# Performance work log

Measured on AMD Instinct MI355X. Metric: run time of the kernel, lower is better.

Reference implementation:

```python
import jax, jax.numpy as jnp
import numpy as np

N, E, C = 100000, 50000, 256
M, D, F, T = 128, 128, 128, 64
MSG = 2 * D + F + T  # 448
T_MAX = 100000


def setup_inputs() -> dict:
    key = jax.random.key(0)
    ks = jax.random.split(key, 16)
    src = jax.random.randint(ks[0], (E,), 0, N, dtype=jnp.int32)
    dst = jax.random.randint(ks[1], (E,), 0, N, dtype=jnp.int32)
    t = jnp.sort(jax.random.randint(ks[2], (E,), 0, T_MAX, dtype=jnp.int32))
    last_update = jax.random.randint(ks[3], (N,), 0, 1000, dtype=jnp.int32)
    event_feat = jax.random.normal(ks[4], (E, F), dtype=jnp.float32)
    src_embeds = jax.random.normal(ks[5], (E, D), dtype=jnp.float32)
    dst_embeds = jax.random.normal(ks[6], (E, D), dtype=jnp.float32)
    nodes_memory = jax.random.normal(ks[7], (N, M), dtype=jnp.float32)
    incidence = jax.random.uniform(ks[8], (N, C), dtype=jnp.float32)
    w_time = jax.random.normal(ks[9], (T,), dtype=jnp.float32)
    b_time = jax.random.normal(ks[10], (T,), dtype=jnp.float32)
    W_ih = jax.random.normal(ks[11], (MSG, 3 * M), dtype=jnp.float32) * 0.05
    W_hh = jax.random.normal(ks[12], (M, 3 * M), dtype=jnp.float32) * 0.05
    b_ih = jnp.zeros((3 * M,), jnp.float32)
    b_hh = jnp.zeros((3 * M,), jnp.float32)
    return dict(src=src, dst=dst, t=t, last_update=last_update,
                event_feat=event_feat, src_embeds=src_embeds, dst_embeds=dst_embeds,
                nodes_memory=nodes_memory, incidence=incidence,
                w_time=w_time, b_time=b_time, W_ih=W_ih, W_hh=W_hh,
                b_ih=b_ih, b_hh=b_hh)


def reference(src, dst, t, last_update, event_feat, src_embeds, dst_embeds,
              nodes_memory, incidence, w_time, b_time, W_ih, W_hh, b_ih, b_hh):
    E2 = 2 * E
    # store_events: raw messages + flipped-direction messages, keyed by source node
    src_all = jnp.concatenate([src, dst])            # [2E]
    emb_s = jnp.concatenate([src_embeds, dst_embeds], axis=0)
    emb_d = jnp.concatenate([dst_embeds, src_embeds], axis=0)
    feat = jnp.concatenate([event_feat, event_feat], axis=0)
    t_all = jnp.concatenate([t, t])                  # [2E]
    # message function: concat(src_embed, dst_embed, event_feat, time_encoding(dt))
    dt = (t_all - last_update[src_all]).astype(jnp.float32)
    time_enc = jnp.cos(dt[:, None] * w_time[None, :] + b_time[None, :])  # [2E, T]
    msg = jnp.concatenate([emb_s, emb_d, feat, time_enc], axis=-1)       # [2E, MSG]
    # 'last' aggregation: per-node argmax over timestamps via rank-encoded segment_max
    perm = jnp.argsort(t_all)  # ascending time order
    rank = jnp.zeros((E2,), jnp.int32).at[perm].set(jnp.arange(E2, dtype=jnp.int32))
    seg_rank = jax.ops.segment_max(rank, src_all, num_segments=N)
    counts = jax.ops.segment_sum(jnp.ones((E2,), jnp.int32), src_all, num_segments=N)
    has_msg = counts > 0                              # [N]
    last_idx = perm[jnp.where(has_msg, seg_rank, 0)]  # [N] event index of last message
    agg_msg = msg[last_idx]                           # [N, MSG]
    # GRU memory updater (torch.nn.GRUCell convention)
    gx = agg_msg @ W_ih + b_ih
    gh = nodes_memory @ W_hh + b_hh
    xr, xz, xn = jnp.split(gx, 3, axis=-1)
    hr, hz, hn = jnp.split(gh, 3, axis=-1)
    r = jax.nn.sigmoid(xr + hr)
    z = jax.nn.sigmoid(xz + hz)
    n = jnp.tanh(xn + r * hn)
    h_new = (1.0 - z) * n + z * nodes_memory
    new_mem = jnp.where(has_msg[:, None], h_new, nodes_memory)  # [N, M]
    # rewire_graph: community memory = incidence.T @ nodes_memory
    comm_mem = jnp.einsum('nc,nm->cm', incidence, new_mem)      # [C, M]
    return jnp.concatenate([new_mem, comm_mem], axis=0)         # [N + C, M]
```

## Files before the change

### kernel.cpp

```cpp
#include <hip/hip_runtime.h>
#include <hip/hip_bf16.h>
#include <stdint.h>

#define N_NODES   100000
#define N_EVENTS  50000
#define N_COMM    256
#define DIM_M     128
#define K_TOT     576
#define GCOLS     512
#define INV2PI    0.15915494309189535f

typedef float f32x4 __attribute__((ext_vector_type(4)));
typedef short s16x8 __attribute__((ext_vector_type(8)));
typedef short s16x4 __attribute__((ext_vector_type(4)));

#define KEYS_OFF   0
#define CNT_OFF    800000
#define LIST_OFF   800008
#define W2PI_OFF   1200128
#define B2PI_OFF   1200384
#define WT_OFF     1200640
#define X_ROWS     100096
#define X_OFF      1790464
#define PART_M_OFF X_OFF
#define CT_NCH     256
#define CT_CPN     392
#define TMP2_OFF   (PART_M_OFF + 33554432)
#define TENC_OFF   1790464
#define PART_F_OFF 14594560

__device__ inline unsigned short f2bf(float x) {
    union { float f; unsigned u; } v; v.f = x;
    unsigned r = v.u + 0x7FFFu + ((v.u >> 16) & 1u);
    return (unsigned short)(r >> 16);
}
__device__ inline float bf2f(unsigned short u) {
    union { unsigned u; float f; } v; v.u = ((unsigned)u) << 16;
    return v.f;
}
__device__ inline float cos_rev(float rev) {
    float fr = rev - floorf(rev);
#if __has_builtin(__builtin_amdgcn_cosf)
    return __builtin_amdgcn_cosf(fr);
#else
    return cosf(fr * 6.283185307179586f);
#endif
}
__device__ inline float sigmoid_f(float x) { return 1.0f / (1.0f + __expf(-x)); }
__device__ inline float tanh_f(float x) {
    float t = __expf(2.0f * x);
    return 1.0f - 2.0f / (t + 1.0f);
}

__global__ __launch_bounds__(256) void k_agg(const int* __restrict__ src,
                                             const int* __restrict__ dst,
                                             const int* __restrict__ t,
                                             unsigned long long* __restrict__ keys) {
    int i = blockIdx.x * 256 + threadIdx.x;
    if (i >= 2 * N_EVENTS) return;
    int e = (i < N_EVENTS) ? i : i - N_EVENTS;
    int node = (i < N_EVENTS) ? src[i] : dst[e];
    unsigned long long key =
        ((unsigned long long)(unsigned)t[e] << 32) | (unsigned)(i + 1);
    atomicMax(&keys[node], key);
}

__global__ __launch_bounds__(256) void k_compact(const unsigned long long* __restrict__ keys,
                                                 unsigned int* __restrict__ cnt,
                                                 int* __restrict__ list) {
    int n = blockIdx.x * 256 + threadIdx.x;
    if (n >= N_NODES) return;
    if (keys[n] != 0ULL) {
        unsigned p = atomicAdd(cnt, 1u);
        list[p] = n;
    }
}

__global__ void k_prep(const float* __restrict__ w_time, const float* __restrict__ b_time,
                       float* __restrict__ w2, float* __restrict__ b2) {
    int i = threadIdx.x;
    if (i < 64) { w2[i] = w_time[i] * INV2PI; b2[i] = b_time[i] * INV2PI; }
}

__global__ __launch_bounds__(256) void k_wconv(const float* __restrict__ W_ih,
                                               const float* __restrict__ W_hh,
                                               unsigned short* __restrict__ Wt) {
    int idx = blockIdx.x * 256 + threadIdx.x;
    if (idx >= GCOLS * K_TOT) return;
    int col2 = idx / K_TOT, k = idx % K_TOT;
    int mh = col2 >> 8, rem = col2 & 255;
    int g = rem >> 6, m = mh * 64 + (rem & 63);
    float v;
    if (g == 0)      v = (k < 448) ? W_ih[(size_t)k * 384 + m]
                                   : W_hh[(size_t)(k - 448) * 384 + m];
    else if (g == 1) v = (k < 448) ? W_ih[(size_t)k * 384 + 128 + m]
                                   : W_hh[(size_t)(k - 448) * 384 + 128 + m];
    else if (g == 2) v = (k < 448) ? W_ih[(size_t)k * 384 + 256 + m] : 0.0f;
    else             v = (k < 448) ? 0.0f : W_hh[(size_t)(k - 448) * 384 + 256 + m];
    Wt[idx] = f2bf(v);
}

__global__ __launch_bounds__(256) void k_wconv_old(const float* __restrict__ W_ih,
                                                   const float* __restrict__ W_hh,
                                                   unsigned short* __restrict__ Wt) {
    int idx = blockIdx.x * 256 + threadIdx.x;
    if (idx >= GCOLS * K_TOT) return;
    int col = idx / K_TOT, k = idx % K_TOT;
    float v;
    if (col < 256) {
        v = (k < 448) ? W_ih[(size_t)k * 384 + col]
                      : W_hh[(size_t)(k - 448) * 384 + col];
    } else if (col < 384) {
        v = (k < 448) ? W_ih[(size_t)k * 384 + col] : 0.0f;
    } else {
        v = (k < 448) ? 0.0f : W_hh[(size_t)(k - 448) * 384 + (col - 128)];
    }
    Wt[idx] = f2bf(v);
}

__global__ __launch_bounds__(256) void k_xbuild(
    const unsigned long long* __restrict__ keys,
    const unsigned int* __restrict__ cnt,
    const int* __restrict__ list,
    const int* __restrict__ t,
    const int* __restrict__ last_update,
    const float* __restrict__ event_feat,
    const float* __restrict__ src_embeds,
    const float* __restrict__ dst_embeds,
    const float* __restrict__ mem,
    const float* __restrict__ w2pi,
    const float* __restrict__ b2pi,
    unsigned short* __restrict__ X) {
    const unsigned c = *cnt;
    const unsigned cpad = (c + 127u) & ~127u;
    const unsigned total = cpad * 72u;
    for (unsigned idx = blockIdx.x * 256 + threadIdx.x; idx < total;
         idx += gridDim.x * 256) {
        const unsigned row = idx / 72u;
        const int s = (int)(idx - row * 72u);
        unsigned short* xp = X + (size_t)row * K_TOT + s * 8;
        s16x8 v;
        if (row >= c) {
#pragma unroll
            for (int j = 0; j < 8; ++j) v[j] = 0;
            *(s16x8*)xp = v;
            continue;
        }
        const int node = list[row];
        const unsigned long long key = keys[node];
        const int ia = (int)(key & 0xffffffffull) - 1;
        const int e = (ia < N_EVENTS) ? ia : ia - N_EVENTS;
        if (s < 48) {
            const float* p;
            if (s < 16)
                p = ((ia < N_EVENTS) ? src_embeds : dst_embeds) + (size_t)e * 128 + s * 8;
            else if (s < 32)
                p = ((ia < N_EVENTS) ? dst_embeds : src_embeds) + (size_t)e * 128 + (s - 16) * 8;
            else
                p = event_feat + (size_t)e * 128 + (s - 32) * 8;
            float4 a = *(const float4*)p;
            float4 b = *(const float4*)(p + 4);
            v[0] = (short)f2bf(a.x); v[1] = (short)f2bf(a.y);
            v[2] = (short)f2bf(a.z); v[3] = (short)f2bf(a.w);
            v[4] = (short)f2bf(b.x); v[5] = (short)f2bf(b.y);
            v[6] = (short)f2bf(b.z); v[7] = (short)f2bf(b.w);
        } else if (s < 56) {
            const float dt = (float)(t[e] - last_update[node]);
            const int c0 = (s - 48) * 8;
#pragma unroll
            for (int j = 0; j < 8; ++j) {
                float rev = fmaf(dt, w2pi[c0 + j], b2pi[c0 + j]);
                v[j] = (short)f2bf(cos_rev(rev));
            }
        } else {
            const float* p = mem + (size_t)node * 128 + (s - 56) * 8;
            float4 a = *(const float4*)p;
            float4 b = *(const float4*)(p + 4);
            v[0] = (short)f2bf(a.x); v[1] = (short)f2bf(a.y);
            v[2] = (short)f2bf(a.z); v[3] = (short)f2bf(a.w);
            v[4] = (short)f2bf(b.x); v[5] = (short)f2bf(b.y);
            v[6] = (short)f2bf(b.z); v[7] = (short)f2bf(b.w);
        }
        *(s16x8*)xp = v;
    }
}

__global__ __launch_bounds__(512, 4) void k_gemm2(
    const unsigned int* __restrict__ cnt,
    const int* __restrict__ list,
    const unsigned short* __restrict__ X,
    const unsigned short* __restrict__ Wt,
    const float* __restrict__ b_ih,
    const float* __restrict__ b_hh,
    float* __restrict__ out) {
    __shared__ unsigned short Xs[3][128][64];
    __shared__ int Ls[128];

    const unsigned c = *cnt;
    const int rb = blockIdx.x >> 1;
    const int mh = blockIdx.x & 1;
    const int base = rb * 128;
    if ((unsigned)base >= c) return;
    const int tid = threadIdx.x;
    const int w = tid >> 6, l = tid & 63;
    const int lr = l & 15, lk = l >> 4;
    const int wm = w >> 2, wn = w & 3;

    if (tid < 128)
        Ls[tid] = ((unsigned)(base + tid) < c) ? list[base + tid] : 0;

    const int sroff = l >> 3;
    const int sslot = ((l & 7) ^ sroff) << 3;
    const unsigned short* gsrc0 =
        X + (size_t)(base + w * 16 + sroff) * K_TOT + sslot;

    auto stage = [&](int ch, int buf) {
        __builtin_amdgcn_global_load_lds(
            (const __attribute__((address_space(1))) unsigned int*)(gsrc0 + ch * 64),
            (__attribute__((address_space(3))) unsigned int*)&Xs[buf][w * 16][0],
            16, 0, 0);
        __builtin_amdgcn_global_load_lds(
            (const __attribute__((address_space(1))) unsigned int*)(gsrc0 + 8 * K_TOT + ch * 64),
            (__attribute__((address_space(3))) unsigned int*)&Xs[buf][w * 16 + 8][0],
            16, 0, 0);
    };

    f32x4 acc[4][4];
#pragma unroll
    for (int rt = 0; rt < 4; ++rt)
#pragma unroll
        for (int i = 0; i < 4; ++i) acc[rt][i] = (f32x4){0.f, 0.f, 0.f, 0.f};

    stage(0, 0);
    stage(1, 1);
    asm volatile("s_waitcnt vmcnt(2)" ::: "memory");
    __builtin_amdgcn_s_barrier();

    int buf = 0;
    for (int ch = 0; ch < 9; ++ch) {
        __builtin_amdgcn_s_setprio(1);
#pragma unroll
        for (int ks = 0; ks < 2; ++ks) {
            s16x8 a[4];
#pragma unroll
            for (int rt = 0; rt < 4; ++rt) {
                const int r = wm * 64 + rt * 16 + lr;
                const int sl = (ks * 4 + lk) ^ (r & 7);
                a[rt] = *(const s16x8*)&Xs[buf][r][sl << 3];
            }
#pragma unroll
            for (int i = 0; i < 4; ++i) {
                const int col2 = mh * 256 + i * 64 + wn * 16 + lr;
                s16x8 b = *(const s16x8*)&Wt[(size_t)col2 * K_TOT + ch * 64 + ks * 32 + lk * 8];
#pragma unroll
                for (int rt = 0; rt < 4; ++rt)
                    acc[rt][i] = __builtin_amdgcn_mfma_f32_16x16x32_bf16(
                        a[rt], b, acc[rt][i], 0, 0, 0);
            }
        }
        __builtin_amdgcn_s_setprio(0);
        if (ch <= 6) {
            int nbuf = buf + 2; if (nbuf >= 3) nbuf -= 3;
            stage(ch + 2, nbuf);
        }
        if (ch < 8) {
            __builtin_amdgcn_sched_barrier(0);
            if (ch < 7) asm volatile("s_waitcnt vmcnt(2)" ::: "memory");
            else        asm volatile("s_waitcnt vmcnt(0)" ::: "memory");
            __builtin_amdgcn_s_barrier();
            __builtin_amdgcn_sched_barrier(0);
        }
        if (++buf == 3) buf = 0;
    }

    const int mcol = mh * 64 + wn * 16 + lr;
    const float b_r  = b_ih[mcol] + b_hh[mcol];
    const float b_z  = b_ih[128 + mcol] + b_hh[128 + mcol];
    const float b_xn = b_ih[256 + mcol];
    const float b_hn = b_hh[256 + mcol];
    const int hbuf = (mcol < 64) ? 1 : 2;
    const int kk   = (mcol < 64) ? mcol : mcol - 64;
#pragma unroll
    for (int rt = 0; rt < 4; ++rt) {
#pragma unroll
        for (int reg = 0; reg < 4; ++reg) {
            const int r = wm * 64 + rt * 16 + lk * 4 + reg;
            const int grow = base + r;
            if ((unsigned)grow < c) {
                const int node = Ls[r];
                const float h = bf2f(Xs[hbuf][r][(((kk >> 3) ^ (r & 7)) << 3) + (kk & 7)]);
                float rr = sigmoid_f(acc[rt][0][reg] + b_r);
                float zz = sigmoid_f(acc[rt][1][reg] + b_z);
                float nn = tanh_f(acc[rt][2][reg] + b_xn + rr * (acc[rt][3][reg] + b_hn));
                out[(size_t)node * 128 + mcol] = (1.0f - zz) * nn + zz * h;
            }
        }
    }
}

__global__ __launch_bounds__(256) void k_copy(const unsigned long long* __restrict__ keys,
                                              const float* __restrict__ nm,
                                              float* __restrict__ out) {
    int idx = blockIdx.x * 256 + threadIdx.x;
    int n = idx >> 5;
    if (n >= N_NODES) return;
    if (keys[n] != 0ULL) return;
    ((float4*)out)[idx] = ((const float4*)nm)[idx];
}

__global__ __launch_bounds__(512) void k_comm_t(const float* __restrict__ inc,
                                                const float* __restrict__ nm,
                                                float* __restrict__ partials) {
    __shared__ unsigned short T[2][12288];

    const int bid = blockIdx.x;
    const int n0 = bid * CT_CPN;
    const int n1 = min(N_NODES, n0 + CT_CPN);
    const int ng = (n1 - n0 + 31) >> 5;
    const int tid = threadIdx.x;
    const int w = tid >> 6, l = tid & 63;
    const int lr = l & 15, lk = l >> 4;

    float vi[4][4];
    float vm[4][2];

    auto load_chunk = [&](int g) {
        const int nb = n0 + g * 32 + w * 4;
#pragma unroll
        for (int ri = 0; ri < 4; ++ri) {
            const int n = nb + ri;
            const bool ok = n < n1;
#pragma unroll
            for (int j = 0; j < 4; ++j)
                vi[ri][j] = ok ? inc[(size_t)n * N_COMM + l + 64 * j] : 0.0f;
#pragma unroll
            for (int j = 0; j < 2; ++j)
                vm[ri][j] = ok ? nm[(size_t)n * DIM_M + l + 64 * j] : 0.0f;
        }
    };
    auto write_chunk = [&](int buf) {
        unsigned short* bi = &T[buf][0];
#pragma unroll
        for (int j = 0; j < 4; ++j) {
            const int cc = l + 64 * j;
            ushort4 p = make_ushort4(f2bf(vi[0][j]), f2bf(vi[1][j]),
                                     f2bf(vi[2][j]), f2bf(vi[3][j]));
            *(ushort4*)&bi[cc * 32 + ((w ^ (cc & 7)) << 2)] = p;
        }
        unsigned short* bm = &T[buf][8192];
#pragma unroll
        for (int j = 0; j < 2; ++j) {
            const int mm = l + 64 * j;
            ushort4 p = make_ushort4(f2bf(vm[0][j]), f2bf(vm[1][j]),
                                     f2bf(vm[2][j]), f2bf(vm[3][j]));
            *(ushort4*)&bm[mm * 32 + ((w ^ (mm & 7)) << 2)] = p;
        }
    };

    f32x4 acc[2][8];
#pragma unroll
    for (int ct = 0; ct < 2; ++ct)
#pragma unroll
        for (int mt = 0; mt < 8; ++mt) acc[ct][mt] = (f32x4){0.f, 0.f, 0.f, 0.f};

    auto compute_chunk = [&](int buf) {
        const unsigned short* bi = &T[buf][0];
        const unsigned short* bm = &T[buf][8192];
        s16x8 a[2];
#pragma unroll
        for (int ct = 0; ct < 2; ++ct) {
            const int cc = (w * 2 + ct) * 16 + lr;
            s16x4 lo = *(const s16x4*)&bi[cc * 32 + (((lk * 2) ^ (cc & 7)) << 2)];
            s16x4 hi = *(const s16x4*)&bi[cc * 32 + (((lk * 2 + 1) ^ (cc & 7)) << 2)];
            a[ct] = __builtin_shufflevector(lo, hi, 0, 1, 2, 3, 4, 5, 6, 7);
        }
#pragma unroll
        for (int mt = 0; mt < 8; ++mt) {
            const int mm = mt * 16 + lr;
            s16x4 lo = *(const s16x4*)&bm[mm * 32 + (((lk * 2) ^ (mm & 7)) << 2)];
            s16x4 hi = *(const s16x4*)&bm[mm * 32 + (((lk * 2 + 1) ^ (mm & 7)) << 2)];
            s16x8 b = __builtin_shufflevector(lo, hi, 0, 1, 2, 3, 4, 5, 6, 7);
            acc[0][mt] = __builtin_amdgcn_mfma_f32_16x16x32_bf16(a[0], b, acc[0][mt], 0, 0, 0);
            acc[1][mt] = __builtin_amdgcn_mfma_f32_16x16x32_bf16(a[1], b, acc[1][mt], 0, 0, 0);
        }
    };

    load_chunk(0);
    write_chunk(0);
    __syncthreads();
    for (int g = 0; g < ng; ++g) {
        if (g + 1 < ng) load_chunk(g + 1);
        compute_chunk(g & 1);
        if (g + 1 < ng) write_chunk((g + 1) & 1);
        __syncthreads();
    }

    float* p = partials + (size_t)bid * (N_COMM * DIM_M);
#pragma unroll
    for (int ct = 0; ct < 2; ++ct) {
#pragma unroll
        for (int mt = 0; mt < 8; ++mt) {
#pragma unroll
            for (int reg = 0; reg < 4; ++reg) {
                const int cc = (w * 2 + ct) * 16 + lk * 4 + reg;
                p[(size_t)cc * DIM_M + mt * 16 + lr] = acc[ct][mt][reg];
            }
        }
    }
}

__global__ __launch_bounds__(256) void k_comm2a(const float* __restrict__ partials,
                                                float* __restrict__ tmp) {
    const int bid = blockIdx.x;
    const int y = bid >> 5, x = bid & 31;
    const int idx4 = x * 256 + threadIdx.x;
    float4 s = make_float4(0.f, 0.f, 0.f, 0.f);
    for (int ci = 0; ci < CT_NCH / 16; ++ci) {
        float4 v = *(const float4*)&partials[(size_t)(y * (CT_NCH / 16) + ci) * (N_COMM * DIM_M) + idx4 * 4];
        s.x += v.x; s.y += v.y; s.z += v.z; s.w += v.w;
    }
    *(float4*)&tmp[(size_t)y * (N_COMM * DIM_M) + idx4 * 4] = s;
}

__global__ __launch_bounds__(256) void k_comm2b(const float* __restrict__ tmp,
                                                float* __restrict__ out) {
    const int idx4 = blockIdx.x * 256 + threadIdx.x;
    float4 s = make_float4(0.f, 0.f, 0.f, 0.f);
    for (int y = 0; y < 16; ++y) {
        float4 v = *(const float4*)&tmp[(size_t)y * (N_COMM * DIM_M) + idx4 * 4];
        s.x += v.x; s.y += v.y; s.z += v.z; s.w += v.w;
    }
    *(float4*)&out[(size_t)N_NODES * DIM_M + idx4 * 4] = s;
}

__global__ __launch_bounds__(256) void k_tenc(const unsigned long long* __restrict__ keys,
                                              const unsigned int* __restrict__ cnt,
                                              const int* __restrict__ list,
                                              const int* __restrict__ t,
                                              const int* __restrict__ last_update,
                                              const float* __restrict__ w_time,
                                              const float* __restrict__ b_time,
                                              unsigned short* __restrict__ tenc) {
    int idx = blockIdx.x * 256 + threadIdx.x;
    int r = idx >> 3, slot = idx & 7;
    const unsigned c = *cnt;
    const unsigned cpad = (c + 63u) & ~63u;
    if ((unsigned)r >= cpad) return;
    s16x8 v;
    if ((unsigned)r < c) {
        int node = list[r];
        unsigned long long key = keys[node];
        int ia = (int)(key & 0xffffffffull) - 1;
        int e = (ia < N_EVENTS) ? ia : ia - N_EVENTS;
        float dt = (float)(t[e] - last_update[node]);
#pragma unroll
        for (int j = 0; j < 8; ++j) {
            int cix = slot * 8 + j;
            float arg = __fadd_rn(__fmul_rn(dt, w_time[cix]), b_time[cix]);
            v[j] = (short)f2bf(cosf(arg));
        }
    } else {
#pragma unroll
        for (int j = 0; j < 8; ++j) v[j] = 0;
    }
    *(s16x8*)&tenc[(size_t)r * 64 + slot * 8] = v;
}

__global__ __launch_bounds__(256, 2) void k_gemm_fused(
    const unsigned long long* __restrict__ keys,
    const unsigned int* __restrict__ cnt,
    const int* __restrict__ list,
    const float* __restrict__ event_feat,
    const float* __restrict__ src_embeds,
    const float* __restrict__ dst_embeds,
    const float* __restrict__ mem,
    const unsigned short* __restrict__ tenc,
    const unsigned short* __restrict__ Wt,
    const float* __restrict__ b_ih,
    const float* __restrict__ b_hh,
    float* __restrict__ out) {
    __shared__ unsigned short Xs[2][4][64][8];

    const unsigned c = *cnt;
    const int base = blockIdx.x * 64;
    if ((unsigned)base >= c) return;
    const int tid = threadIdx.x;

    const int srow = tid >> 2;
    const int kslot = tid & 3;
    const int sgrow = base + srow;
    const bool valid = (unsigned)sgrow < c;
    const float *p_es = nullptr, *p_ed = nullptr, *p_ef = nullptr, *p_mem = nullptr;
    const unsigned short* p_te = nullptr;
    if (valid) {
        int node = list[sgrow];
        unsigned long long key = keys[node];
        int ia = (int)(key & 0xffffffffull) - 1;
        int e = (ia < N_EVENTS) ? ia : ia - N_EVENTS;
        const float* sp = src_embeds + (size_t)e * 128;
        const float* dp = dst_embeds + (size_t)e * 128;
        p_es = (ia < N_EVENTS) ? sp : dp;
        p_ed = (ia < N_EVENTS) ? dp : sp;
        p_ef = event_feat + (size_t)e * 128;
        p_te = tenc + (size_t)sgrow * 64;
        p_mem = mem + (size_t)node * 128;
    }

    auto stage = [&](int ch) {
        const int buf = ch & 1;
        const int k0 = ch * 32 + kslot * 8;
        s16x8 v;
        if (valid) {
            if (k0 < 384) {
                const float* p = (k0 < 128) ? (p_es + k0)
                               : (k0 < 256) ? (p_ed + (k0 - 128))
                                            : (p_ef + (k0 - 256));
                float4 a = *(const float4*)p;
                float4 b = *(const float4*)(p + 4);
                v[0] = (short)f2bf(a.x); v[1] = (short)f2bf(a.y);
                v[2] = (short)f2bf(a.z); v[3] = (short)f2bf(a.w);
                v[4] = (short)f2bf(b.x); v[5] = (short)f2bf(b.y);
                v[6] = (short)f2bf(b.z); v[7] = (short)f2bf(b.w);
            } else if (k0 < 448) {
                v = *(const s16x8*)(p_te + (k0 - 384));
            } else {
                const float* p = p_mem + (k0 - 448);
                float4 a = *(const float4*)p;
                float4 b = *(const float4*)(p + 4);
                v[0] = (short)f2bf(a.x); v[1] = (short)f2bf(a.y);
                v[2] = (short)f2bf(a.z); v[3] = (short)f2bf(a.w);
                v[4] = (short)f2bf(b.x); v[5] = (short)f2bf(b.y);
                v[6] = (short)f2bf(b.z); v[7] = (short)f2bf(b.w);
            }
        } else {
#pragma unroll
            for (int j = 0; j < 8; ++j) v[j] = 0;
        }
        *(s16x8*)&Xs[buf][kslot][srow][0] = v;
    };

    const int w = tid >> 6;
    const int l = tid & 63;
    const int lr = l & 15;
    const int lk = l >> 4;

    f32x4 acc[4][8];
#pragma unroll
    for (int rt = 0; rt < 4; ++rt)
#pragma unroll
        for (int i = 0; i < 8; ++i) acc[rt][i] = (f32x4){0.f, 0.f, 0.f, 0.f};

    stage(0);
    __syncthreads();

    for (int ch = 0; ch < 18; ++ch) {
        if (ch < 17) stage(ch + 1);
        const int buf = ch & 1;
        s16x8 a[4];
#pragma unroll
        for (int rt = 0; rt < 4; ++rt)
            a[rt] = *(const s16x8*)&Xs[buf][lk][rt * 16 + lr][0];
#pragma unroll
        for (int i = 0; i < 8; ++i) {
            const int col = (w + 4 * i) * 16 + lr;
            s16x8 b = *(const s16x8*)&Wt[(size_t)col * K_TOT + ch * 32 + lk * 8];
#pragma unroll
            for (int rt = 0; rt < 4; ++rt)
                acc[rt][i] = __builtin_amdgcn_mfma_f32_16x16x32_bf16(
                    a[rt], b, acc[rt][i], 0, 0, 0);
        }
        __syncthreads();
    }

#pragma unroll
    for (int jj = 0; jj < 2; ++jj) {
        const int mcol = (w + 4 * jj) * 16 + lr;
        const float b_r  = b_ih[mcol] + b_hh[mcol];
        const float b_z  = b_ih[128 + mcol] + b_hh[128 + mcol];
        const float b_xn = b_ih[256 + mcol];
        const float b_hn = b_hh[256 + mcol];
#pragma unroll
        for (int rt = 0; rt < 4; ++rt) {
#pragma unroll
            for (int reg = 0; reg < 4; ++reg) {
                const int grow = base + rt * 16 + lk * 4 + reg;
                if ((unsigned)grow < c) {
                    const int node = list[grow];
                    const float h = mem[(size_t)node * 128 + mcol];
                    float rr = sigmoid_f(acc[rt][0 + jj][reg] + b_r);
                    float zz = sigmoid_f(acc[rt][2 + jj][reg] + b_z);
                    float nn = tanh_f(acc[rt][4 + jj][reg] + b_xn +
                                      rr * (acc[rt][6 + jj][reg] + b_hn));
                    out[(size_t)node * 128 + mcol] = (1.0f - zz) * nn + zz * h;
                }
            }
        }
    }
}

__global__ __launch_bounds__(256) void k_comm1(const float* __restrict__ inc,
                                               const float* __restrict__ nm,
                                               float* __restrict__ partials,
                                               int nch, int cpn) {
    __shared__ float inc_s[2][8][128];
    __shared__ float mem_s[2][8][128];

    const int bid = blockIdx.x;
    const int ct2 = bid / nch;
    const int ch  = bid % nch;
    const int n0 = ch * cpn;
    const int n1 = min(N_NODES, n0 + cpn);
    const int tid = threadIdx.x;

    const int srow = tid >> 5;
    const int scol = (tid & 31) * 4;

    auto stage = [&](int g, int buf) {
        const int n = n0 + g * 8 + srow;
        float4 iv = make_float4(0.f, 0.f, 0.f, 0.f);
        float4 mv = make_float4(0.f, 0.f, 0.f, 0.f);
        if (n < n1) {
            iv = *(const float4*)(inc + (size_t)n * N_COMM + ct2 * 128 + scol);
            mv = *(const float4*)(nm + (size_t)n * DIM_M + scol);
        }
        *(float4*)&inc_s[buf][srow][scol] = iv;
        *(float4*)&mem_s[buf][srow][scol] = mv;
    };

    const int c0 = (tid >> 3) * 4;
    const int mb = (tid & 7) * 4;

    float acc[4][4][4];
#pragma unroll
    for (int a = 0; a < 4; ++a)
#pragma unroll
        for (int b = 0; b < 4; ++b)
#pragma unroll
            for (int d = 0; d < 4; ++d) acc[a][b][d] = 0.0f;

    const int ngrp = (n1 - n0 + 7) >> 3;
    stage(0, 0);
    __syncthreads();

    for (int g = 0; g < ngrp; ++g) {
        if (g + 1 < ngrp) stage(g + 1, (g + 1) & 1);
        const int buf = g & 1;
#pragma unroll
        for (int i = 0; i < 8; ++i) {
            const float4 cv = *(const float4*)&inc_s[buf][i][c0];
            const float ca[4] = {cv.x, cv.y, cv.z, cv.w};
#pragma unroll
            for (int j = 0; j < 4; ++j) {
                const float4 mv = *(const float4*)&mem_s[buf][i][j * 32 + mb];
                const float ma[4] = {mv.x, mv.y, mv.z, mv.w};
#pragma unroll
                for (int ci = 0; ci < 4; ++ci)
#pragma unroll
                    for (int mi = 0; mi < 4; ++mi)
                        acc[ci][j][mi] = fmaf(ca[ci], ma[mi], acc[ci][j][mi]);
            }
        }
        __syncthreads();
    }

    float* p = partials + (size_t)bid * (128 * 128);
#pragma unroll
    for (int ci = 0; ci < 4; ++ci)
#pragma unroll
        for (int j = 0; j < 4; ++j)
            *(float4*)(p + (size_t)(c0 + ci) * 128 + j * 32 + mb) =
                make_float4(acc[ci][j][0], acc[ci][j][1], acc[ci][j][2], acc[ci][j][3]);
}

__global__ __launch_bounds__(256) void k_comm2_f(const float* __restrict__ partials,
                                                 float* __restrict__ out,
                                                 int nch) {
    int idx = blockIdx.x * 256 + threadIdx.x;
    if (idx >= N_COMM * DIM_M) return;
    int cg = idx >> 7;
    int m = idx & 127;
    int ct2 = cg >> 7;
    int cl = cg & 127;
    float s = 0.0f;
    for (int ch = 0; ch < nch; ++ch)
        s += partials[((size_t)ct2 * nch + ch) * 16384 + (size_t)cl * 128 + m];
    out[(size_t)N_NODES * DIM_M + idx] = s;
}

extern "C" void kernel_launch(void* const* d_in, const int* in_sizes, int n_in,
                              void* d_out, int out_size, void* d_ws, size_t ws_size,
                              hipStream_t stream) {
    const int* src          = (const int*)d_in[0];
    const int* dst          = (const int*)d_in[1];
    const int* t            = (const int*)d_in[2];
    const int* last_update  = (const int*)d_in[3];
    const float* event_feat = (const float*)d_in[4];
    const float* src_embeds = (const float*)d_in[5];
    const float* dst_embeds = (const float*)d_in[6];
    const float* nodes_mem  = (const float*)d_in[7];
    const float* incidence  = (const float*)d_in[8];
    const float* w_time     = (const float*)d_in[9];
    const float* b_time     = (const float*)d_in[10];
    const float* W_ih       = (const float*)d_in[11];
    const float* W_hh       = (const float*)d_in[12];
    const float* b_ih       = (const float*)d_in[13];
    const float* b_hh       = (const float*)d_in[14];
    float* out = (float*)d_out;

    char* ws = (char*)d_ws;
    unsigned long long* keys = (unsigned long long*)(ws + KEYS_OFF);
    unsigned int* cnt        = (unsigned int*)(ws + CNT_OFF);
    int* list                = (int*)(ws + LIST_OFF);
    float* w2pi              = (float*)(ws + W2PI_OFF);
    float* b2pi              = (float*)(ws + B2PI_OFF);
    unsigned short* Wt       = (unsigned short*)(ws + WT_OFF);

    const bool xfit = ws_size >= (size_t)X_OFF + (size_t)X_ROWS * (K_TOT * 2);

    hipMemsetAsync(d_ws, 0, LIST_OFF, stream);

    k_agg<<<(2 * N_EVENTS + 255) / 256, 256, 0, stream>>>(src, dst, t, keys);
    k_compact<<<(N_NODES + 255) / 256, 256, 0, stream>>>(keys, cnt, list);
    k_prep<<<1, 64, 0, stream>>>(w_time, b_time, w2pi, b2pi);

    if (xfit) {
        unsigned short* X = (unsigned short*)(ws + X_OFF);
        float* partials   = (float*)(ws + PART_M_OFF);
        float* tmp2       = (float*)(ws + TMP2_OFF);

        k_wconv<<<(GCOLS * K_TOT + 255) / 256, 256, 0, stream>>>(W_ih, W_hh, Wt);
        k_xbuild<<<4096, 256, 0, stream>>>(keys, cnt, list, t, last_update,
                                           event_feat, src_embeds, dst_embeds,
                                           nodes_mem, w2pi, b2pi, X);
        k_gemm2<<<(X_ROWS / 128) * 2, 512, 0, stream>>>(cnt, list, X, Wt, b_ih, b_hh, out);
        k_copy<<<(N_NODES * 32 + 255) / 256, 256, 0, stream>>>(keys, nodes_mem, out);
        k_comm_t<<<CT_NCH, 512, 0, stream>>>(incidence, out, partials);
        k_comm2a<<<512, 256, 0, stream>>>(partials, tmp2);
        k_comm2b<<<32, 256, 0, stream>>>(tmp2, out);
    } else {
        unsigned short* tenc = (unsigned short*)(ws + TENC_OFF);
        float* partials      = (float*)(ws + PART_F_OFF);
        int NCH = 512;
        while (NCH > 8 && (size_t)PART_F_OFF + (size_t)NCH * 131072 > ws_size) NCH >>= 1;
        int cpn = (N_NODES + NCH - 1) / NCH;

        k_wconv_old<<<(GCOLS * K_TOT + 255) / 256, 256, 0, stream>>>(W_ih, W_hh, Wt);
        k_tenc<<<(100032 * 8) / 256, 256, 0, stream>>>(keys, cnt, list, t, last_update,
                                                       w_time, b_time, tenc);
        k_gemm_fused<<<100032 / 64, 256, 0, stream>>>(keys, cnt, list, event_feat,
                                                      src_embeds, dst_embeds, nodes_mem,
                                                      tenc, Wt, b_ih, b_hh, out);
        k_copy<<<(N_NODES * 32 + 255) / 256, 256, 0, stream>>>(keys, nodes_mem, out);
        k_comm1<<<2 * NCH, 256, 0, stream>>>(incidence, out, partials, NCH, cpn);
        k_comm2_f<<<(N_COMM * DIM_M + 255) / 256, 256, 0, stream>>>(partials, out, NCH);
    }
}
```

Measured before the change: 232.7 us.

## Stage GRU weight tiles into LDS alongside activations in gemm kernel

The GEMM kernel now copies the weight (Wt) tiles into a triple-buffered shared-memory array with asynchronous global-to-LDS loads and the same XOR swizzle used for activations. Each wave used to read its B fragments straight from global memory for every MFMA; now the block loads them once and every wave reads them from LDS. The prefetch of chunk ch+2 is issued before the compute instead of after it, the loop is fully unrolled, and the wait counts are adjusted for six loads per stage. The cost is much more shared memory per block (about 147KB), which likely allows only one block per CU and lowers occupancy.

```diff
diff --git a/kernel.cpp b/kernel.cpp
--- a/kernel.cpp
+++ b/kernel.cpp
@@ -193,7 +193,8 @@
     const float* __restrict__ b_ih,
     const float* __restrict__ b_hh,
     float* __restrict__ out) {
-    __shared__ unsigned short Xs[3][128][64];
+    __shared__ unsigned short As[3][128][64];
+    __shared__ unsigned short Bs[3][256][64];
     __shared__ int Ls[128];
 
     const unsigned c = *cnt;
@@ -209,20 +210,24 @@
     if (tid < 128)
         Ls[tid] = ((unsigned)(base + tid) < c) ? list[base + tid] : 0;
 
-    const int sroff = l >> 3;
-    const int sslot = ((l & 7) ^ sroff) << 3;
-    const unsigned short* gsrc0 =
-        X + (size_t)(base + w * 16 + sroff) * K_TOT + sslot;
+    const int r8 = tid >> 3;
+    const int sj = tid & 7;
+    const int srcsl = (sj ^ (r8 & 7)) << 3;
+    const unsigned short* gA0 = X + (size_t)(base + r8) * K_TOT + srcsl;
+    const unsigned short* gA1 = X + (size_t)(base + 64 + r8) * K_TOT + srcsl;
+    const unsigned short* gB0 = Wt + (size_t)(mh * 256 + r8) * K_TOT + srcsl;
+
+#define GLD(SRC, DST) __builtin_amdgcn_global_load_lds( \
+        (const __attribute__((address_space(1))) unsigned int*)(SRC), \
+        (__attribute__((address_space(3))) unsigned int*)(DST), 16, 0, 0)
 
     auto stage = [&](int ch, int buf) {
-        __builtin_amdgcn_global_load_lds(
-            (const __attribute__((address_space(1))) unsigned int*)(gsrc0 + ch * 64),
-            (__attribute__((address_space(3))) unsigned int*)&Xs[buf][w * 16][0],
-            16, 0, 0);
-        __builtin_amdgcn_global_load_lds(
-            (const __attribute__((address_space(1))) unsigned int*)(gsrc0 + 8 * K_TOT + ch * 64),
-            (__attribute__((address_space(3))) unsigned int*)&Xs[buf][w * 16 + 8][0],
-            16, 0, 0);
+        GLD(gA0 + ch * 64, &As[buf][w * 8][0]);
+        GLD(gA1 + ch * 64, &As[buf][64 + w * 8][0]);
+        GLD(gB0 + ch * 64,                          &Bs[buf][w * 8][0]);
+        GLD(gB0 + (size_t)64 * K_TOT + ch * 64,     &Bs[buf][64 + w * 8][0]);
+        GLD(gB0 + (size_t)128 * K_TOT + ch * 64,    &Bs[buf][128 + w * 8][0]);
+        GLD(gB0 + (size_t)192 * K_TOT + ch * 64,    &Bs[buf][192 + w * 8][0]);
     };
 
     f32x4 acc[4][4];
@@ -233,11 +238,12 @@
 
     stage(0, 0);
     stage(1, 1);
-    asm volatile("s_waitcnt vmcnt(2)" ::: "memory");
-    __builtin_amdgcn_s_barrier();
-
-    int buf = 0;
+    __syncthreads();
+
+#pragma unroll
     for (int ch = 0; ch < 9; ++ch) {
+        const int buf = ch % 3;
+        if (ch <= 6) stage(ch + 2, (ch + 2) % 3);
         __builtin_amdgcn_s_setprio(1);
 #pragma unroll
         for (int ks = 0; ks < 2; ++ks) {
@@ -246,12 +252,13 @@
             for (int rt = 0; rt < 4; ++rt) {
                 const int r = wm * 64 + rt * 16 + lr;
                 const int sl = (ks * 4 + lk) ^ (r & 7);
-                a[rt] = *(const s16x8*)&Xs[buf][r][sl << 3];
+                a[rt] = *(const s16x8*)&As[buf][r][sl << 3];
             }
 #pragma unroll
             for (int i = 0; i < 4; ++i) {
-                const int col2 = mh * 256 + i * 64 + wn * 16 + lr;
-                s16x8 b = *(const s16x8*)&Wt[(size_t)col2 * K_TOT + ch * 64 + ks * 32 + lk * 8];
+                const int col = i * 64 + wn * 16 + lr;
+                const int slb = (ks * 4 + lk) ^ (col & 7);
+                s16x8 b = *(const s16x8*)&Bs[buf][col][slb << 3];
 #pragma unroll
                 for (int rt = 0; rt < 4; ++rt)
                     acc[rt][i] = __builtin_amdgcn_mfma_f32_16x16x32_bf16(
@@ -259,18 +266,13 @@
             }
         }
         __builtin_amdgcn_s_setprio(0);
-        if (ch <= 6) {
-            int nbuf = buf + 2; if (nbuf >= 3) nbuf -= 3;
-            stage(ch + 2, nbuf);
-        }
         if (ch < 8) {
             __builtin_amdgcn_sched_barrier(0);
-            if (ch < 7) asm volatile("s_waitcnt vmcnt(2)" ::: "memory");
+            if (ch < 7) asm volatile("s_waitcnt vmcnt(6)" ::: "memory");
             else        asm volatile("s_waitcnt vmcnt(0)" ::: "memory");
             __builtin_amdgcn_s_barrier();
             __builtin_amdgcn_sched_barrier(0);
         }
-        if (++buf == 3) buf = 0;
     }
 
     const int mcol = mh * 64 + wn * 16 + lr;
@@ -288,7 +290,7 @@
             const int grow = base + r;
             if ((unsigned)grow < c) {
                 const int node = Ls[r];
-                const float h = bf2f(Xs[hbuf][r][(((kk >> 3) ^ (r & 7)) << 3) + (kk & 7)]);
+                const float h = bf2f(As[hbuf][r][(((kk >> 3) ^ (r & 7)) << 3) + (kk & 7)]);
                 float rr = sigmoid_f(acc[rt][0][reg] + b_r);
                 float zz = sigmoid_f(acc[rt][1][reg] + b_z);
                 float nn = tanh_f(acc[rt][2][reg] + b_xn + rr * (acc[rt][3][reg] + b_hn));
@@ -296,6 +298,7 @@
             }
         }
     }
+#undef GLD
 }
 
 __global__ __launch_bounds__(256) void k_copy(const unsigned long long* __restrict__ keys,
```

After: 203.0 us. -12.8%, faster.
